# Optimization experiments

Measured on AMD Instinct MI355X. Metric: run time of the kernel, lower is better.

The kernel has to match this reference:

```python
import jax, jax.numpy as jnp
import numpy as np

EPS = 1e-05
NEG = -1e9

def rotate_half(x):
    x1, x2 = jnp.split(x, 2, axis=-1)
    return jnp.concatenate([-x2, x1], axis=-1)

def rmsnorm(x, w):
    xf = x.astype(jnp.float32)
    n = xf * jax.lax.rsqrt(jnp.mean(xf * xf, axis=-1, keepdims=True) + EPS)
    return w * n.astype(x.dtype)

def setup_inputs() -> dict:
    key = jax.random.key(0)
    ks = jax.random.split(key, 12)
    B, S, H, NH, DH, FF = 1, 2048, 2048, 16, 128, 8192
    x = jax.random.normal(ks[0], (B, S, H), jnp.float32)
    # additive causal mask [1,1,S,S]
    causal = jnp.where(jnp.tril(jnp.ones((S, S), bool)), 0.0, NEG).astype(jnp.float32)
    attention_mask = causal[None, None]
    alibi = 0.1 * jax.random.normal(ks[1], (1, NH, S, S), jnp.float32)
    # rotary angles [S, DH]
    inv = 1.0 / (10000.0 ** (jnp.arange(0, DH, 2, dtype=jnp.float32) / DH))
    ang = jnp.arange(S, dtype=jnp.float32)[:, None] * inv[None, :]
    freqs = jnp.concatenate([ang, ang], axis=-1)  # [S, DH]
    sc = 1.0 / np.sqrt(H)
    wq = sc * jax.random.normal(ks[2], (H, H), jnp.float32)
    wk = sc * jax.random.normal(ks[3], (H, H), jnp.float32)
    wv = sc * jax.random.normal(ks[4], (H, H), jnp.float32)
    wo = sc * jax.random.normal(ks[5], (H, H), jnp.float32)
    w1 = sc * jax.random.normal(ks[6], (H, FF), jnp.float32)
    w3 = sc * jax.random.normal(ks[7], (H, FF), jnp.float32)
    w2 = (1.0 / np.sqrt(FF)) * jax.random.normal(ks[8], (FF, H), jnp.float32)
    attn_norm_w = jnp.ones((H,), jnp.float32)
    ffn_norm_w = jnp.ones((H,), jnp.float32)
    return dict(x=x, attention_mask=attention_mask, alibi=alibi, freqs=freqs,
                wq=wq, wk=wk, wv=wv, wo=wo, w1=w1, w2=w2, w3=w3,
                attn_norm_w=attn_norm_w, ffn_norm_w=ffn_norm_w)

def reference(x, attention_mask, alibi, freqs, wq, wk, wv, wo, w1, w2, w3,
              attn_norm_w, ffn_norm_w):
    B, S, H = x.shape
    NH = 16
    DH = H // NH
    nx = rmsnorm(x, attn_norm_w)
    # projections -> [B, NH, S, DH]
    def heads(y):
        return y.reshape(B, S, NH, DH).transpose(0, 2, 1, 3)
    q = heads(nx @ wq)
    k = heads(nx @ wk)
    v = heads(nx @ wv)
    cos, sin = jnp.cos(freqs), jnp.sin(freqs)  # [S, DH] broadcasts over B,NH
    q = q * cos + rotate_half(q) * sin
    k = k * cos + rotate_half(k) * sin
    scores = jnp.einsum('bhqd,bhkd->bhqk', q, k) / np.sqrt(DH)
    scores = scores + attention_mask + alibi
    attn = jax.nn.softmax(scores, axis=-1)
    out = jnp.einsum('bhqk,bhkd->bhqd', attn, v)
    out = out.transpose(0, 2, 1, 3).reshape(B, S, H)
    x = x + out @ wo
    nx = rmsnorm(x, ffn_norm_w)
    ff = (jax.nn.silu(nx @ w1) * (nx @ w3)) @ w2
    return x + ff
```

## Files before the change

### kernel.cpp

```cpp
#include <hip/hip_runtime.h>
#include <hip/hip_bf16.h>
#include <math.h>

typedef __bf16 bf16x8 __attribute__((ext_vector_type(8)));
typedef float  f32x4  __attribute__((ext_vector_type(4)));
typedef unsigned short u16x8 __attribute__((ext_vector_type(8)));

#define DEV static __device__ __forceinline__

DEV void gload16(const void* g, void* l) {
  __builtin_amdgcn_global_load_lds((__attribute__((address_space(1))) void*)g,
                                   (__attribute__((address_space(3))) void*)l,
                                   16, 0, 0);
}

DEV float bf2f(unsigned short u) {
  unsigned v = ((unsigned)u) << 16;
  return __builtin_bit_cast(float, v);
}
DEV unsigned short f2bf(float f) {
  unsigned u = __builtin_bit_cast(unsigned, f);
  u = u + 0x7fffu + ((u >> 16) & 1u);
  return (unsigned short)(u >> 16);
}

__global__ __launch_bounds__(256) void rmsnorm_k(const float* __restrict__ x,
    const float* __restrict__ w, unsigned short* __restrict__ out, int H) {
  int row = blockIdx.x;
  const float4* xr = (const float4*)(x + (size_t)row * H);
  float4 a = xr[threadIdx.x * 2], b = xr[threadIdx.x * 2 + 1];
  float ss = a.x*a.x + a.y*a.y + a.z*a.z + a.w*a.w
           + b.x*b.x + b.y*b.y + b.z*b.z + b.w*b.w;
#pragma unroll
  for (int o = 32; o; o >>= 1) ss += __shfl_down(ss, o, 64);
  __shared__ float red[4];
  if ((threadIdx.x & 63) == 0) red[threadIdx.x >> 6] = ss;
  __syncthreads();
  float rs = rsqrtf((red[0] + red[1] + red[2] + red[3]) * (1.0f / 2048.0f) + 1e-5f);
  size_t base = (size_t)row * H + threadIdx.x * 8;
  const float* wv = w + threadIdx.x * 8;
  float vals[8] = {a.x, a.y, a.z, a.w, b.x, b.y, b.z, b.w};
  u16x8 o8;
#pragma unroll
  for (int i = 0; i < 8; ++i) o8[i] = f2bf(vals[i] * rs * wv[i]);
  *(u16x8*)(out + base) = o8;
}

__global__ __launch_bounds__(256) void wtrans_k(const float* __restrict__ W,
    unsigned short* __restrict__ Wt, int R, int C) {
  __shared__ float tile[32][33];
  int c0 = blockIdx.x * 32, r0 = blockIdx.y * 32;
  int tx = threadIdx.x, ty = threadIdx.y;
#pragma unroll
  for (int i = 0; i < 4; ++i)
    tile[ty + i * 8][tx] = W[(size_t)(r0 + ty + i * 8) * C + c0 + tx];
  __syncthreads();
#pragma unroll
  for (int i = 0; i < 4; ++i)
    Wt[(size_t)(c0 + ty + i * 8) * R + r0 + tx] = f2bf(tile[tx][ty + i * 8]);
}

__global__ __launch_bounds__(256) void wtrans_ilv_k(const float* __restrict__ W,
    unsigned short* __restrict__ Wt, int R, int C, int half) {
  __shared__ float tile[32][33];
  int c0 = blockIdx.x * 32, r0 = blockIdx.y * 32;
  int tx = threadIdx.x, ty = threadIdx.y;
#pragma unroll
  for (int i = 0; i < 4; ++i)
    tile[ty + i * 8][tx] = W[(size_t)(r0 + ty + i * 8) * C + c0 + tx];
  __syncthreads();
#pragma unroll
  for (int i = 0; i < 4; ++i) {
    int c = c0 + ty + i * 8;
    size_t dstrow = (size_t)(c >> 4) * 32 + (c & 15) + half * 16;
    Wt[dstrow * R + r0 + tx] = f2bf(tile[tx][ty + i * 8]);
  }
}


#define STG_A(H, BUF, KC) do {                                                 \
    gload16(Asrc0 + (size_t)(H) * 128 * lda + (KC),                            \
            &lds[(BUF) * 16384 + (H) * 8192 + w * 1024]);                      \
    gload16(Asrc1 + (size_t)(H) * 128 * lda + (KC),                            \
            &lds[(BUF) * 16384 + (H) * 8192 + w * 1024 + 512]);                \
  } while (0)

#define STG_B(H, BUF, KC) do {                                                 \
    gload16(Bsrc0 + (size_t)(H) * 128 * ldb + (KC),                            \
            &lds[32768 + (BUF) * 16384 + (H) * 8192 + w * 1024]);              \
    gload16(Bsrc1 + (size_t)(H) * 128 * ldb + (KC),                            \
            &lds[32768 + (BUF) * 16384 + (H) * 8192 + w * 1024 + 512]);        \
  } while (0)

#define DS_A(DST, MH) do {                                                     \
    const int abase = buf * 16384 + (MH) * 8192 + arow * 64;                   \
    _Pragma("unroll") for (int m = 0; m < 4; ++m) {                            \
      DST[m][0] = *(const bf16x8*)&lds[abase + m * 1024 + acol0];              \
      DST[m][1] = *(const bf16x8*)&lds[abase + m * 1024 + acol1];              \
    } } while (0)

#define DS_B(DST, NH) do {                                                     \
    const int bbase = 32768 + buf * 16384 + (NH) * 8192 + brow * 64;           \
    _Pragma("unroll") for (int n = 0; n < 2; ++n) {                            \
      DST[n][0] = *(const bf16x8*)&lds[bbase + n * 1024 + acol0];              \
      DST[n][1] = *(const bf16x8*)&lds[bbase + n * 1024 + acol1];              \
    } } while (0)

#define MFMA16(AI, AR, BR) do {                                                \
    __builtin_amdgcn_s_setprio(1);                                             \
    _Pragma("unroll") for (int m = 0; m < 4; ++m)                              \
      _Pragma("unroll") for (int n = 0; n < 2; ++n) {                          \
        acc[AI][m][n] = __builtin_amdgcn_mfma_f32_16x16x32_bf16(               \
            AR[m][0], BR[n][0], acc[AI][m][n], 0, 0, 0);                       \
        acc[AI][m][n] = __builtin_amdgcn_mfma_f32_16x16x32_bf16(               \
            AR[m][1], BR[n][1], acc[AI][m][n], 0, 0, 0);                       \
      }                                                                        \
    __builtin_amdgcn_s_setprio(0);                                             \
    __builtin_amdgcn_sched_barrier(0);                                         \
  } while (0)

#define SBAR_WAIT do {                                                         \
    __builtin_amdgcn_sched_barrier(0);                                         \
    __builtin_amdgcn_s_barrier();                                              \
    asm volatile("s_waitcnt lgkmcnt(0)" ::: "memory");                         \
  } while (0)

template <int EPI>
__global__ __launch_bounds__(512, 2) void gemm256_k(
    const unsigned short* __restrict__ A, int lda,
    const unsigned short* __restrict__ B, int ldb,
    unsigned short* __restrict__ Cb, float* __restrict__ Cf,
    int M, int N, int Kext) {
  __shared__ unsigned short lds[65536];
  const int t = threadIdx.x, w = t >> 6, lane = t & 63;
  const int nbm = M >> 8, nbn = N >> 8, nwg = nbm * nbn;
  int id = blockIdx.x;
  id = (id & 7) * (nwg >> 3) + (id >> 3);
  const int bm = id % nbm, bn = id / nbm;
  const size_t m0 = (size_t)bm << 8, n0 = (size_t)bn << 8;
  const int koff = blockIdx.y * Kext;
  const int NT = Kext >> 6;
  const int scol = ((lane & 7) ^ (lane >> 3)) * 8;
  const unsigned short* Asrc0 = A + (m0 + w * 16 + (lane >> 3)) * (size_t)lda + koff + scol;
  const unsigned short* Asrc1 = A + (m0 + w * 16 + 8 + (lane >> 3)) * (size_t)lda + koff + scol;
  const unsigned short* Bsrc0 = B + (n0 + w * 16 + (lane >> 3)) * (size_t)ldb + koff + scol;
  const unsigned short* Bsrc1 = B + (n0 + w * 16 + 8 + (lane >> 3)) * (size_t)ldb + koff + scol;
  const int arow = (w >> 2) * 64 + (lane & 15);
  const int brow = (w & 3) * 32 + (lane & 15);
  const int acol0 = ((lane >> 4) * 8) ^ ((lane & 7) << 3);
  const int acol1 = acol0 ^ 32;
  f32x4 acc[4][4][2] = {};
  bf16x8 Acur[4][2], B0r[2][2], B1r[2][2];
  STG_A(0, 0, 0); STG_B(0, 0, 0); STG_A(1, 0, 0); STG_B(1, 0, 0);
  STG_A(0, 1, 64); STG_B(0, 1, 64);
  asm volatile("s_waitcnt vmcnt(4)" ::: "memory");
  __builtin_amdgcn_s_barrier();
  for (int kt = 0; kt < NT; ++kt) {
    const int buf = kt & 1;
    const int kc1 = (kt + 1) * 64, kc2 = (kt + 2) * 64;
    const bool p1 = (kt + 1 < NT), p2 = (kt + 2 < NT);
    DS_A(Acur, 0); DS_B(B0r, 0);
    if (p1) STG_A(1, buf ^ 1, kc1);
    SBAR_WAIT;
    MFMA16(0, Acur, B0r);
    __builtin_amdgcn_s_barrier();
    DS_B(B1r, 1);
    if (p1) STG_B(1, buf ^ 1, kc1);
    SBAR_WAIT;
    MFMA16(1, Acur, B1r);
    __builtin_amdgcn_s_barrier();
    DS_A(Acur, 1);
    if (p2) STG_A(0, buf, kc2);
    SBAR_WAIT;
    MFMA16(3, Acur, B1r);
    __builtin_amdgcn_s_barrier();
    if (p2) STG_B(0, buf, kc2);
    __builtin_amdgcn_sched_barrier(0);
    __builtin_amdgcn_s_barrier();
    MFMA16(2, Acur, B0r);
    if (p2) { asm volatile("s_waitcnt vmcnt(4)" ::: "memory"); }
    else    { asm volatile("s_waitcnt vmcnt(0)" ::: "memory"); }
    __builtin_amdgcn_s_barrier();
  }
#pragma unroll
  for (int Mh = 0; Mh < 2; ++Mh)
#pragma unroll
    for (int Nh = 0; Nh < 2; ++Nh)
#pragma unroll
      for (int m = 0; m < 4; ++m) {
        size_t gr = m0 + Mh * 128 + (w >> 2) * 64 + m * 16 + (lane >> 4) * 4;
        if constexpr (EPI == 2) {
          size_t gc = (n0 >> 1) + Nh * 64 + (w & 3) * 16 + (lane & 15);
          f32x4 v0 = acc[Mh * 2 + Nh][m][0];
          f32x4 v1 = acc[Mh * 2 + Nh][m][1];
#pragma unroll
          for (int j = 0; j < 4; ++j) {
            float s = v0[j] / (1.0f + __expf(-v0[j]));
            Cb[(gr + j) * (size_t)(N >> 1) + gc] = f2bf(s * v1[j]);
          }
        } else {
#pragma unroll
          for (int n = 0; n < 2; ++n) {
            size_t gc = n0 + Nh * 128 + (w & 3) * 32 + n * 16 + (lane & 15);
            f32x4 v = acc[Mh * 2 + Nh][m][n];
#pragma unroll
            for (int j = 0; j < 4; ++j) {
              size_t o = (gr + j) * (size_t)N + gc;
              if constexpr (EPI == 0) Cb[o] = f2bf(v[j]);
              else Cf[(size_t)blockIdx.y * M * N + o] = v[j];
            }
          }
        }
      }
}

template <int EPI>
__global__ __launch_bounds__(256) void gemm_bt_k(
    const unsigned short* __restrict__ A, const unsigned short* __restrict__ B,
    float* __restrict__ Cf, unsigned short* __restrict__ Cb,
    const float* __restrict__ resid, int M, int N, int K) {
  constexpr int BK = 64;
  __shared__ unsigned short lA[128 * BK];
  __shared__ unsigned short lB[128 * BK];
  const int t = threadIdx.x, wave = t >> 6, lane = t & 63;
  int nwg = gridDim.x * gridDim.y;
  int id = blockIdx.y * gridDim.x + blockIdx.x;
  id = (id & 7) * (nwg >> 3) + (id >> 3);
  const int m0 = (id % gridDim.x) * 128, n0 = (id / gridDim.x) * 128;
  const int wr = (wave >> 1) * 64, wc = (wave & 1) * 64;
  f32x4 acc[4][4] = {};
  const int sr = t >> 3;
  const int sc = ((t & 7) ^ (sr & 7)) * 8;
  const unsigned short* Ab = A + (size_t)(m0 + sr) * K + sc;
  const unsigned short* Bb = B + (size_t)(n0 + sr) * K + sc;
  unsigned short* lAw = &lA[(wave * 8) * BK];
  unsigned short* lBw = &lB[(wave * 8) * BK];
  const int row = lane & 15, kg = (lane >> 4) * 8, swz = (lane & 7) << 3;
  for (int k0 = 0; k0 < K; k0 += BK) {
#pragma unroll
    for (int it = 0; it < 4; ++it) {
      gload16(Ab + (size_t)it * 32 * K + k0, lAw + it * 32 * BK);
      gload16(Bb + (size_t)it * 32 * K + k0, lBw + it * 32 * BK);
    }
    asm volatile("s_waitcnt vmcnt(0)" ::: "memory");
    __syncthreads();
#pragma unroll
    for (int kk = 0; kk < 2; ++kk) {
      bf16x8 af[4], bfr[4];
#pragma unroll
      for (int m = 0; m < 4; ++m)
        af[m] = *(const bf16x8*)&lA[(wr + m * 16 + row) * BK + ((kk * 32 + kg) ^ swz)];
#pragma unroll
      for (int n = 0; n < 4; ++n)
        bfr[n] = *(const bf16x8*)&lB[(wc + n * 16 + row) * BK + ((kk * 32 + kg) ^ swz)];
#pragma unroll
      for (int m = 0; m < 4; ++m)
#pragma unroll
        for (int n = 0; n < 4; ++n)
          acc[m][n] = __builtin_amdgcn_mfma_f32_16x16x32_bf16(af[m], bfr[n], acc[m][n], 0, 0, 0);
    }
    __syncthreads();
  }
  const int cg = lane >> 4, col = lane & 15;
#pragma unroll
  for (int m = 0; m < 4; ++m)
#pragma unroll
    for (int n = 0; n < 4; ++n) {
      int rr = m0 + wr + m * 16 + cg * 4;
      int cc = n0 + wc + n * 16 + col;
#pragma unroll
      for (int j = 0; j < 4; ++j) {
        float v = acc[m][n][j];
        size_t o = (size_t)(rr + j) * N + cc;
        if constexpr (EPI == 2) Cf[o] = v + resid[o];
        else if constexpr (EPI == 1) Cf[o] = v;
        else Cb[o] = f2bf(v);
      }
    }
}

__global__ __launch_bounds__(256) void rope_k(const unsigned short* __restrict__ qkv,
    const float* __restrict__ freqs, unsigned short* __restrict__ Qr,
    unsigned short* __restrict__ Kr, int S) {
  int idx = blockIdx.x * 256 + threadIdx.x;
  int dp = idx & 63, h = (idx >> 6) & 15, s = idx >> 10;
  float ang = freqs[s * 128 + dp];
  float c, sn;
  sincosf(ang, &sn, &c);
  size_t rq = (size_t)s * 6144 + h * 128 + dp;
  float q1 = bf2f(qkv[rq]),        q2 = bf2f(qkv[rq + 64]);
  float k1 = bf2f(qkv[rq + 2048]), k2 = bf2f(qkv[rq + 2048 + 64]);
  size_t ob = ((size_t)h * S + s) * 128 + dp;
  Qr[ob]      = f2bf(q1 * c - q2 * sn);
  Qr[ob + 64] = f2bf(q2 * c + q1 * sn);
  Kr[ob]      = f2bf(k1 * c - k2 * sn);
  Kr[ob + 64] = f2bf(k2 * c + k1 * sn);
}

__global__ __launch_bounds__(256) void vtrans_k(const unsigned short* __restrict__ qkv,
    unsigned short* __restrict__ Vt, int S) {
  __shared__ unsigned short tile[32][33];
  int h = blockIdx.z;
  int s0 = blockIdx.x * 32, d0 = blockIdx.y * 32;
  int tx = threadIdx.x, ty = threadIdx.y;
#pragma unroll
  for (int i = 0; i < 4; ++i)
    tile[ty + i * 8][tx] = qkv[(size_t)(s0 + ty + i * 8) * 6144 + 4096 + h * 128 + d0 + tx];
  __syncthreads();
#pragma unroll
  for (int i = 0; i < 4; ++i)
    Vt[((size_t)h * 128 + d0 + ty + i * 8) * S + s0 + tx] = tile[tx][ty + i * 8];
}


#define STGKV(KT, BUF) do {                                                    \
    _Pragma("unroll") for (int it = 0; it < 4; ++it)                           \
      gload16(Kb + (size_t)((KT) * 64 + it * 16 + sr) * 128 + scw,             \
              &lds[(BUF) * 8192 + (it * 16 + wave * 4) * 128]);                \
    _Pragma("unroll") for (int it = 0; it < 4; ++it)                           \
      gload16(Vb + (size_t)(it * 32 + vr) * S + (KT) * 64 + vcw,               \
              &lds[16384 + (BUF) * 8192 + (it * 32 + wave * 8) * 64]);         \
  } while (0)

#define ATTN_TILE(CUR, NXT, KT) do {                                           \
    const int buf = (KT) & 1;                                                  \
    const bool p1 = ((KT) + 1 < ktiles);                                       \
    if (p1) {                                                                  \
      STGKV((KT) + 1, buf ^ 1);                                                \
      _Pragma("unroll") for (int q8 = 0; q8 < 16; ++q8)                        \
        NXT[q8] = albase[(size_t)(q8 & 3) * S + ((KT) + 1) * 64 + (q8 >> 2) * 16]; \
      asm volatile("s_waitcnt vmcnt(24)" ::: "memory");                        \
    } else {                                                                   \
      asm volatile("s_waitcnt vmcnt(0)" ::: "memory");                         \
    }                                                                          \
    __builtin_amdgcn_s_barrier();                                              \
    f32x4 sf[4] = {};                                                          \
    _Pragma("unroll") for (int ks = 0; ks < 4; ++ks)                           \
      _Pragma("unroll") for (int n = 0; n < 4; ++n) {                          \
        bf16x8 kf = *(const bf16x8*)&lds[buf * 8192 + (n * 16 + row) * 128 +   \
                                         ((ks * 32 + kg) ^ kswz)];             \
        sf[n] = __builtin_amdgcn_mfma_f32_16x16x32_bf16(qf[ks], kf, sf[n], 0, 0, 0); \
      }                                                                        \
    float pv[4][4];                                                            \
    float tmax[4] = {-1e30f, -1e30f, -1e30f, -1e30f};                          \
    _Pragma("unroll") for (int n = 0; n < 4; ++n) {                            \
      int k_abs = (KT) * 64 + n * 16 + col;                                    \
      _Pragma("unroll") for (int j = 0; j < 4; ++j) {                          \
        int q_abs = q0 + wave * 16 + cg * 4 + j;                               \
        float v = sf[n][j] * scale + CUR[n * 4 + j];                           \
        if (k_abs > q_abs) v = -1e30f;                                         \
        pv[n][j] = v;                                                          \
        tmax[j] = fmaxf(tmax[j], v);                                           \
      } }                                                                      \
    _Pragma("unroll") for (int o2 = 1; o2 < 16; o2 <<= 1)                      \
      _Pragma("unroll") for (int j = 0; j < 4; ++j)                            \
        tmax[j] = fmaxf(tmax[j], __shfl_xor(tmax[j], o2, 64));                 \
    float alpha[4], rsum[4] = {};                                              \
    _Pragma("unroll") for (int j = 0; j < 4; ++j) {                            \
      float mn = fmaxf(m_run[j], tmax[j]);                                     \
      alpha[j] = __expf(m_run[j] - mn);                                        \
      m_run[j] = mn;                                                           \
    }                                                                          \
    _Pragma("unroll") for (int n = 0; n < 4; ++n)                              \
      _Pragma("unroll") for (int j = 0; j < 4; ++j) {                          \
        float p = __expf(pv[n][j] - m_run[j]);                                 \
        pv[n][j] = p;                                                          \
        rsum[j] += p;                                                          \
      }                                                                        \
    _Pragma("unroll") for (int o2 = 1; o2 < 16; o2 <<= 1)                      \
      _Pragma("unroll") for (int j = 0; j < 4; ++j)                            \
        rsum[j] += __shfl_xor(rsum[j], o2, 64);                                \
    _Pragma("unroll") for (int j = 0; j < 4; ++j)                              \
      l_run[j] = l_run[j] * alpha[j] + rsum[j];                                \
    _Pragma("unroll") for (int nn = 0; nn < 8; ++nn)                           \
      _Pragma("unroll") for (int j = 0; j < 4; ++j) o[nn][j] *= alpha[j];      \
    _Pragma("unroll") for (int n = 0; n < 4; ++n)                              \
      _Pragma("unroll") for (int j = 0; j < 4; ++j) {                          \
        int pr = cg * 4 + j;                                                   \
        pw[pr * 64 + ((n * 16 + col) ^ ((pr & 7) << 3))] = f2bf(pv[n][j]);     \
      }                                                                        \
    asm volatile("s_waitcnt lgkmcnt(0)" ::: "memory");                         \
    __builtin_amdgcn_sched_barrier(0);                                         \
    _Pragma("unroll") for (int kk = 0; kk < 2; ++kk) {                         \
      bf16x8 pf = *(const bf16x8*)&pw[row * 64 + ((kk * 32 + kg) ^ kswz)];     \
      _Pragma("unroll") for (int nn = 0; nn < 8; ++nn) {                       \
        bf16x8 vf = *(const bf16x8*)&lds[16384 + buf * 8192 +                  \
                                         (nn * 16 + row) * 64 +                \
                                         ((kk * 32 + kg) ^ kswz)];             \
        o[nn] = __builtin_amdgcn_mfma_f32_16x16x32_bf16(pf, vf, o[nn], 0, 0, 0); \
      } }                                                                      \
    __builtin_amdgcn_s_barrier();                                              \
  } while (0)

__global__ __launch_bounds__(256) void attn_k(
    const unsigned short* __restrict__ Qr, const unsigned short* __restrict__ Kr,
    const unsigned short* __restrict__ Vt, const float* __restrict__ alibi,
    unsigned short* __restrict__ Ao, int S) {
  __shared__ unsigned short lds[36864];
  const int t = threadIdx.x, wave = t >> 6, lane = t & 63;
  const int h = blockIdx.y, nq = gridDim.x, bx = blockIdx.x;
  const int qt = (bx & 1) ? (nq - 1 - (bx >> 1)) : (bx >> 1);
  const int q0 = qt * 64;
  const int sr = t >> 4, scw = ((t & 15) ^ ((t >> 4) & 7)) * 8;
  const int vr = t >> 3, vcw = ((t & 7) ^ ((t >> 3) & 7)) * 8;
  const unsigned short* Kb = Kr + (size_t)h * S * 128;
  const unsigned short* Vb = Vt + (size_t)h * 128 * S;
  const int row = lane & 15, kg = (lane >> 4) * 8, cg = lane >> 4, col = lane & 15;
  const int kswz = (lane & 7) << 3;
  bf16x8 qf[4];
  const unsigned short* Qrow = Qr + ((size_t)h * S + q0 + wave * 16 + row) * 128;
#pragma unroll
  for (int ks = 0; ks < 4; ++ks) qf[ks] = *(const bf16x8*)&Qrow[ks * 32 + kg];
  f32x4 o[8] = {};
  float m_run[4] = {-1e30f, -1e30f, -1e30f, -1e30f};
  float l_run[4] = {};
  unsigned short* pw = &lds[32768 + wave * 1024];
  const float scale = 0.08838834764831843f;
  const int ktiles = qt + 1;
  const float* albase = alibi + (size_t)h * S * S +
                        ((size_t)q0 + wave * 16 + cg * 4) * S + col;
  float alA[16], alB[16];
  STGKV(0, 0);
#pragma unroll
  for (int q8 = 0; q8 < 16; ++q8)
    alA[q8] = albase[(size_t)(q8 & 3) * S + (q8 >> 2) * 16];
  for (int kt = 0; kt < ktiles; kt += 2) {
    ATTN_TILE(alA, alB, kt);
    if (kt + 1 < ktiles) ATTN_TILE(alB, alA, kt + 1);
  }
#pragma unroll
  for (int nn = 0; nn < 8; ++nn)
#pragma unroll
    for (int j = 0; j < 4; ++j) {
      int q_abs = q0 + wave * 16 + cg * 4 + j;
      Ao[(size_t)q_abs * 2048 + h * 128 + nn * 16 + col] = f2bf(o[nn][j] / l_run[j]);
    }
}

__global__ __launch_bounds__(256) void reduce4_k(const float* __restrict__ part,
    const float* __restrict__ resid, float* __restrict__ out, int n4, size_t mn) {
  int i = blockIdx.x * 256 + threadIdx.x;
  if (i >= n4) return;
  const float4* p = (const float4*)part;
  size_t q = mn >> 2;
  float4 a = ((const float4*)resid)[i];
  float4 s0 = p[i], s1 = p[i + q], s2 = p[i + 2 * q], s3 = p[i + 3 * q];
  float4 r;
  r.x = a.x + s0.x + s1.x + s2.x + s3.x;
  r.y = a.y + s0.y + s1.y + s2.y + s3.y;
  r.z = a.z + s0.z + s1.z + s2.z + s3.z;
  r.w = a.w + s0.w + s1.w + s2.w + s3.w;
  ((float4*)out)[i] = r;
}

extern "C" void kernel_launch(void* const* d_in, const int* in_sizes, int n_in,
                              void* d_out, int out_size, void* d_ws, size_t ws_size,
                              hipStream_t stream) {
  const int S = 2048, H = 2048, NH = 16, DH = 128, FF = 8192;
  const float* x     = (const float*)d_in[0];
  const float* alibi = (const float*)d_in[2];
  const float* freqs = (const float*)d_in[3];
  const float* wq    = (const float*)d_in[4];
  const float* wk    = (const float*)d_in[5];
  const float* wv    = (const float*)d_in[6];
  const float* wo    = (const float*)d_in[7];
  const float* w1    = (const float*)d_in[8];
  const float* w2    = (const float*)d_in[9];
  const float* w3    = (const float*)d_in[10];
  const float* anw   = (const float*)d_in[11];
  const float* fnw   = (const float*)d_in[12];
  float* out = (float*)d_out;

  char* ws = (char*)d_ws;
  size_t off = 0;
  auto alloc = [&](size_t n) { char* p = ws + off; off += (n + 255) & ~(size_t)255; return p; };
  unsigned short* qkvT = (unsigned short*)alloc((size_t)3 * H * H * 2);
  unsigned short* woT  = (unsigned short*)alloc((size_t)H * H * 2);
  unsigned short* w13T = (unsigned short*)alloc((size_t)2 * FF * H * 2);
  unsigned short* w2T  = (unsigned short*)alloc((size_t)H * FF * 2);
  float*          x2   = (float*)alloc((size_t)S * H * 4);
  unsigned short* nx2  = (unsigned short*)alloc((size_t)S * H * 2);
  unsigned short* gbuf = (unsigned short*)alloc((size_t)S * FF * 2);
  unsigned short* nx   = (unsigned short*)alloc((size_t)S * H * 2);
  unsigned short* qkvb = (unsigned short*)alloc((size_t)S * 3 * H * 2);
  unsigned short* Qr   = (unsigned short*)alloc((size_t)NH * S * DH * 2);
  unsigned short* Kr   = (unsigned short*)alloc((size_t)NH * S * DH * 2);
  unsigned short* Vt   = (unsigned short*)alloc((size_t)NH * DH * S * 2);
  unsigned short* attno= (unsigned short*)alloc((size_t)S * H * 2);
  float* part = (float*)ws;

  dim3 tb32(32, 8);
  wtrans_k<<<dim3(64, 64), tb32, 0, stream>>>(wq, qkvT, H, H);
  wtrans_k<<<dim3(64, 64), tb32, 0, stream>>>(wk, qkvT + (size_t)H * H, H, H);
  wtrans_k<<<dim3(64, 64), tb32, 0, stream>>>(wv, qkvT + (size_t)2 * H * H, H, H);
  wtrans_k<<<dim3(64, 64), tb32, 0, stream>>>(wo, woT, H, H);
  wtrans_ilv_k<<<dim3(256, 64), tb32, 0, stream>>>(w1, w13T, H, FF, 0);
  wtrans_ilv_k<<<dim3(256, 64), tb32, 0, stream>>>(w3, w13T, H, FF, 1);
  wtrans_k<<<dim3(64, 256), tb32, 0, stream>>>(w2, w2T, FF, H);

  rmsnorm_k<<<S, 256, 0, stream>>>(x, anw, nx, H);
  gemm256_k<0><<<dim3(192, 1), 512, 0, stream>>>(nx, H, qkvT, H, qkvb, nullptr, S, 3 * H, H);
  rope_k<<<(S * NH * 64) / 256, 256, 0, stream>>>(qkvb, freqs, Qr, Kr, S);
  vtrans_k<<<dim3(S / 32, DH / 32, NH), tb32, 0, stream>>>(qkvb, Vt, S);
  attn_k<<<dim3(S / 64, NH), 256, 0, stream>>>(Qr, Kr, Vt, alibi, attno, S);
  gemm_bt_k<2><<<dim3(16, 16), 256, 0, stream>>>(attno, woT, x2, nullptr, x, S, H, H);
  rmsnorm_k<<<S, 256, 0, stream>>>(x2, fnw, nx2, H);
  gemm256_k<2><<<dim3(512, 1), 512, 0, stream>>>(nx2, H, w13T, H, gbuf, nullptr, S, 2 * FF, H);
  gemm256_k<1><<<dim3(64, 4), 512, 0, stream>>>(gbuf, FF, w2T, FF, nullptr, part, S, H, H);
  reduce4_k<<<4096, 256, 0, stream>>>(part, x2, out, S * H / 4, (size_t)S * H);
}
```

Measured before the change: 545.2 us.

## Vectorize weight transpose with 64x64 bf16 tiles and drop GEMM lgkmcnt waits

Merges the two weight-transpose kernels into one 64x64-tile kernel. It loads float4, converts to bf16 before staging in LDS, and writes 16-byte vectors, which cuts the per-element global traffic in the per-call weight preprocessing. Separately, the GEMM main loop drops the explicit s_waitcnt lgkmcnt(0) after each barrier and the sched_barrier after the MFMA blocks. That leaves LDS-read waits to the compiler, which could allow more overlap but changes the hand-tuned ordering.

```diff
diff --git a/kernel.cpp b/kernel.cpp
--- a/kernel.cpp
+++ b/kernel.cpp
@@ -5,6 +5,7 @@
 typedef __bf16 bf16x8 __attribute__((ext_vector_type(8)));
 typedef float  f32x4  __attribute__((ext_vector_type(4)));
 typedef unsigned short u16x8 __attribute__((ext_vector_type(8)));
+typedef unsigned short u16x4 __attribute__((ext_vector_type(4)));
 
 #define DEV static __device__ __forceinline__
 
@@ -46,34 +47,30 @@
   *(u16x8*)(out + base) = o8;
 }
 
-__global__ __launch_bounds__(256) void wtrans_k(const float* __restrict__ W,
-    unsigned short* __restrict__ Wt, int R, int C) {
-  __shared__ float tile[32][33];
-  int c0 = blockIdx.x * 32, r0 = blockIdx.y * 32;
-  int tx = threadIdx.x, ty = threadIdx.y;
-#pragma unroll
-  for (int i = 0; i < 4; ++i)
-    tile[ty + i * 8][tx] = W[(size_t)(r0 + ty + i * 8) * C + c0 + tx];
+__global__ __launch_bounds__(256) void wtrans64_k(const float* __restrict__ W,
+    unsigned short* __restrict__ Wt, int R, int C, int ilv) {
+  __shared__ unsigned short tile[64][68];
+  const int c0 = blockIdx.x * 64, r0 = blockIdx.y * 64;
+  const int t = threadIdx.x;
+  const int lr = t >> 4, lc4 = (t & 15) * 4;
+#pragma unroll
+  for (int i = 0; i < 4; ++i) {
+    float4 v = *(const float4*)&W[(size_t)(r0 + lr + i * 16) * C + c0 + lc4];
+    u16x4 s4;
+    s4[0] = f2bf(v.x); s4[1] = f2bf(v.y); s4[2] = f2bf(v.z); s4[3] = f2bf(v.w);
+    *(u16x4*)&tile[lr + i * 16][lc4] = s4;
+  }
   __syncthreads();
-#pragma unroll
-  for (int i = 0; i < 4; ++i)
-    Wt[(size_t)(c0 + ty + i * 8) * R + r0 + tx] = f2bf(tile[tx][ty + i * 8]);
-}
-
-__global__ __launch_bounds__(256) void wtrans_ilv_k(const float* __restrict__ W,
-    unsigned short* __restrict__ Wt, int R, int C, int half) {
-  __shared__ float tile[32][33];
-  int c0 = blockIdx.x * 32, r0 = blockIdx.y * 32;
-  int tx = threadIdx.x, ty = threadIdx.y;
-#pragma unroll
-  for (int i = 0; i < 4; ++i)
-    tile[ty + i * 8][tx] = W[(size_t)(r0 + ty + i * 8) * C + c0 + tx];
-  __syncthreads();
-#pragma unroll
-  for (int i = 0; i < 4; ++i) {
-    int c = c0 + ty + i * 8;
-    size_t dstrow = (size_t)(c >> 4) * 32 + (c & 15) + half * 16;
-    Wt[dstrow * R + r0 + tx] = f2bf(tile[tx][ty + i * 8]);
+  const int oc = t >> 3, seg = (t & 7) * 8;
+#pragma unroll
+  for (int i = 0; i < 2; ++i) {
+    int c = c0 + oc + i * 32;
+    u16x8 o8;
+#pragma unroll
+    for (int j = 0; j < 8; ++j) o8[j] = tile[seg + j][oc + i * 32];
+    size_t dstrow = (ilv < 0) ? (size_t)c
+                              : (size_t)(c >> 4) * 32 + (c & 15) + ilv * 16;
+    *(u16x8*)&Wt[dstrow * R + r0 + seg] = o8;
   }
 }
 
@@ -116,13 +113,6 @@
             AR[m][1], BR[n][1], acc[AI][m][n], 0, 0, 0);                       \
       }                                                                        \
     __builtin_amdgcn_s_setprio(0);                                             \
-    __builtin_amdgcn_sched_barrier(0);                                         \
-  } while (0)
-
-#define SBAR_WAIT do {                                                         \
-    __builtin_amdgcn_sched_barrier(0);                                         \
-    __builtin_amdgcn_s_barrier();                                              \
-    asm volatile("s_waitcnt lgkmcnt(0)" ::: "memory");                         \
   } while (0)
 
 template <int EPI>
@@ -161,17 +151,20 @@
     const bool p1 = (kt + 1 < NT), p2 = (kt + 2 < NT);
     DS_A(Acur, 0); DS_B(B0r, 0);
     if (p1) STG_A(1, buf ^ 1, kc1);
-    SBAR_WAIT;
+    __builtin_amdgcn_sched_barrier(0);
+    __builtin_amdgcn_s_barrier();
     MFMA16(0, Acur, B0r);
     __builtin_amdgcn_s_barrier();
     DS_B(B1r, 1);
     if (p1) STG_B(1, buf ^ 1, kc1);
-    SBAR_WAIT;
+    __builtin_amdgcn_sched_barrier(0);
+    __builtin_amdgcn_s_barrier();
     MFMA16(1, Acur, B1r);
     __builtin_amdgcn_s_barrier();
     DS_A(Acur, 1);
     if (p2) STG_A(0, buf, kc2);
-    SBAR_WAIT;
+    __builtin_amdgcn_sched_barrier(0);
+    __builtin_amdgcn_s_barrier();
     MFMA16(3, Acur, B1r);
     __builtin_amdgcn_s_barrier();
     if (p2) STG_B(0, buf, kc2);
@@ -311,7 +304,6 @@
   for (int i = 0; i < 4; ++i)
     Vt[((size_t)h * 128 + d0 + ty + i * 8) * S + s0 + tx] = tile[tx][ty + i * 8];
 }
-
 
 #define STGKV(KT, BUF) do {                                                    \
     _Pragma("unroll") for (int it = 0; it < 4; ++it)                           \
@@ -490,13 +482,13 @@
   float* part = (float*)ws;
 
   dim3 tb32(32, 8);
-  wtrans_k<<<dim3(64, 64), tb32, 0, stream>>>(wq, qkvT, H, H);
-  wtrans_k<<<dim3(64, 64), tb32, 0, stream>>>(wk, qkvT + (size_t)H * H, H, H);
-  wtrans_k<<<dim3(64, 64), tb32, 0, stream>>>(wv, qkvT + (size_t)2 * H * H, H, H);
-  wtrans_k<<<dim3(64, 64), tb32, 0, stream>>>(wo, woT, H, H);
-  wtrans_ilv_k<<<dim3(256, 64), tb32, 0, stream>>>(w1, w13T, H, FF, 0);
-  wtrans_ilv_k<<<dim3(256, 64), tb32, 0, stream>>>(w3, w13T, H, FF, 1);
-  wtrans_k<<<dim3(64, 256), tb32, 0, stream>>>(w2, w2T, FF, H);
+  wtrans64_k<<<dim3(32, 32), 256, 0, stream>>>(wq, qkvT, H, H, -1);
+  wtrans64_k<<<dim3(32, 32), 256, 0, stream>>>(wk, qkvT + (size_t)H * H, H, H, -1);
+  wtrans64_k<<<dim3(32, 32), 256, 0, stream>>>(wv, qkvT + (size_t)2 * H * H, H, H, -1);
+  wtrans64_k<<<dim3(32, 32), 256, 0, stream>>>(wo, woT, H, H, -1);
+  wtrans64_k<<<dim3(128, 32), 256, 0, stream>>>(w1, w13T, H, FF, 0);
+  wtrans64_k<<<dim3(128, 32), 256, 0, stream>>>(w3, w13T, H, FF, 1);
+  wtrans64_k<<<dim3(32, 128), 256, 0, stream>>>(w2, w2T, FF, H, -1);
 
   rmsnorm_k<<<S, 256, 0, stream>>>(x, anw, nx, H);
   gemm256_k<0><<<dim3(192, 1), 512, 0, stream>>>(nx, H, qkvT, H, qkvb, nullptr, S, 3 * H, H);
```

Measured after the change: 537.2 us. About the same (-1.5%).
